# Kernel tuning notes

Measured on AMD Instinct MI355X. Metric: run time of the kernel, lower is better.

## Reference

```python
import jax, jax.numpy as jnp
import numpy as np

INF = 1e38  # matches torch module's INF = 1e+38


def setup_inputs() -> dict:
    key = jax.random.key(0)
    k1, k2, k3 = jax.random.split(key, 3)
    n_len, batch, dim = 2048, 4, 512
    # scale query so QK^T logits don't fully saturate the softmax
    query = jax.random.normal(k1, (n_len, batch, dim), dtype=jnp.float32) * 0.05
    W_in = jax.random.normal(k2, (dim, dim), dtype=jnp.float32) * (1.0 / np.sqrt(dim))
    W_out = jax.random.normal(k3, (dim, 2 * dim), dtype=jnp.float32) * (1.0 / np.sqrt(2 * dim))
    return {"query": query, "W_in": W_in, "W_out": W_out}


def reference(query, W_in, W_out):
    # query: [n_len, batch, dim]; torch .t() swaps first two dims -> [batch, n_len, dim]
    q = jnp.transpose(query, (1, 0, 2))
    b, n, d = q.shape
    # attention_type == 'general': linear_in (no bias), y = x @ W^T
    q = jnp.einsum('bnd,ed->bne', q, W_in)
    # scores: [b, n, n]
    scores = jnp.einsum('bnd,bmd->bnm', q, q)
    # mask = triu(ones) INCLUDING diagonal -> set to -INF (row 0 fully masked)
    mask = jnp.triu(jnp.ones((n, n), dtype=bool))
    scores = jnp.where(mask[None, :, :], -INF, scores)
    weights = jax.nn.softmax(scores, axis=-1)  # row 0 becomes uniform (all -INF)
    # manual zero-out of row 0 of the attention weights
    weights = weights.at[:, 0, :].set(0.0)
    mix = jnp.einsum('bnm,bmd->bnd', weights, q)
    combined = jnp.concatenate([mix, q], axis=-1)  # [b, n, 2d]
    out = jnp.einsum('bnk,dk->bnd', combined, W_out)  # linear_out, no bias
    out = jax.nn.selu(out)
    # final .t() -> [n_len, batch, dim]
    return jnp.transpose(out, (1, 0, 2)), weights
```

## Files before the change

### kernel.cpp

```cpp
#include <hip/hip_runtime.h>
#include <hip/hip_bf16.h>

typedef unsigned short u16;
typedef unsigned int u32;

#define BATCH 4
#define NLEN 2048
#define DIM 512
#define LDSK 40

typedef __attribute__((ext_vector_type(8))) __bf16 bf16x8;
typedef __attribute__((ext_vector_type(4))) float f32x4;

typedef const __attribute__((address_space(1))) void gv_t;
typedef __attribute__((address_space(3))) void lv_t;

__device__ __forceinline__ u16 f32_to_bf16(float f) {
  union { float f; u32 u; } v; v.f = f;
  u32 u = v.u;
  return (u16)((u + 0x7FFFu + ((u >> 16) & 1u)) >> 16);
}
__device__ __forceinline__ u32 pk2(float lo, float hi) {
  return (u32)f32_to_bf16(lo) | ((u32)f32_to_bf16(hi) << 16);
}
__device__ __forceinline__ void stage8_f32(u16* dst, const float* src) {
  float4 a = *(const float4*)src;
  float4 b = *(const float4*)(src + 4);
  uint4 o;
  o.x = pk2(a.x, a.y); o.y = pk2(a.z, a.w);
  o.z = pk2(b.x, b.y); o.w = pk2(b.z, b.w);
  *(uint4*)dst = o;
}
__device__ __forceinline__ void stage16_f32(u16* dst, const float* src) {
  stage8_f32(dst, src); stage8_f32(dst + 8, src + 8);
}
__device__ __forceinline__ u32 addpk_bf16(u32 a, u32 b) {
  float a0 = __uint_as_float(a << 16), a1 = __uint_as_float(a & 0xffff0000u);
  float b0 = __uint_as_float(b << 16), b1 = __uint_as_float(b & 0xffff0000u);
  return pk2(a0 + b0, a1 + b1);
}

template <int NRPW>
__device__ __forceinline__ void glds_rows(const u16* gsrc, size_t gstride, u16* lds,
                                          int wrow0, int lane) {
  const int r = lane >> 3;
  const int c = (lane & 7) * 8;
#pragma unroll
  for (int i = 0; i < NRPW; i += 8) {
    const int row = wrow0 + i + r;
    __builtin_amdgcn_global_load_lds((gv_t*)(gsrc + (size_t)row * gstride + c),
                                     (lv_t*)(lds + row * 64 + c), 16, 0, 0);
  }
}

__global__ __launch_bounds__(256) void k_qproj(const float* __restrict__ query,
                                               const float* __restrict__ W_in,
                                               u16* __restrict__ qp, u16* __restrict__ qt) {
  __shared__ u16 As[64 * LDSK];
  __shared__ u16 Bs[128 * LDSK];
  __shared__ u16 tbuf[128][72];
  const int t = threadIdx.x;
  const int lane = t & 63, wid = t >> 6;
  const int wm = (wid >> 1) * 32, wn = (wid & 1) * 64;
  const int lr = lane & 15, lk = (lane >> 4) * 8;
  const int trow4 = t >> 2, tseg = (t & 3) * 8;
  const int trow2 = t >> 1, thalf = (t & 1) * 16;
  const int rbase = blockIdx.y * 64;
  const int cbase = blockIdx.x * 128;
  const int rg = rbase + trow4;
  const int bb = rg >> 11, nn = rg & 2047;
  const float* aRow = query + (size_t)(nn * BATCH + bb) * DIM + tseg;
  const float* bRow = W_in + (size_t)(cbase + trow2) * DIM + thalf;
  f32x4 acc[2][4] = {};
  for (int k0 = 0; k0 < DIM; k0 += 32) {
    stage8_f32(As + trow4 * LDSK + tseg, aRow + k0);
    stage16_f32(Bs + trow2 * LDSK + thalf, bRow + k0);
    __syncthreads();
    bf16x8 af[2], bfr[4];
#pragma unroll
    for (int m = 0; m < 2; ++m) af[m] = *(const bf16x8*)(As + (wm + m * 16 + lr) * LDSK + lk);
#pragma unroll
    for (int n = 0; n < 4; ++n) bfr[n] = *(const bf16x8*)(Bs + (wn + n * 16 + lr) * LDSK + lk);
#pragma unroll
    for (int m = 0; m < 2; ++m)
#pragma unroll
      for (int n = 0; n < 4; ++n)
        acc[m][n] = __builtin_amdgcn_mfma_f32_16x16x32_bf16(af[m], bfr[n], acc[m][n], 0, 0, 0);
    __syncthreads();
  }
#pragma unroll
  for (int m = 0; m < 2; ++m)
#pragma unroll
    for (int n = 0; n < 4; ++n)
#pragma unroll
      for (int j = 0; j < 4; ++j) {
        int rl = wm + m * 16 + (lane >> 4) * 4 + j;
        int cl = wn + n * 16 + lr;
        u16 v = f32_to_bf16(acc[m][n][j]);
        qp[(size_t)(rbase + rl) * DIM + cbase + cl] = v;
        tbuf[cl][rl] = v;
      }
  __syncthreads();
  const int bb0 = rbase >> 11, nbase = rbase & 2047;
#pragma unroll
  for (int i = 0; i < 4; ++i) {
    int idx = t + i * 256;
    int dl = idx >> 3, c = idx & 7;
    uint4 v = *(const uint4*)&tbuf[dl][c * 8];
    *(uint4*)(qt + (size_t)(bb0 * DIM + cbase + dl) * NLEN + nbase + c * 8) = v;
  }
}

__global__ __launch_bounds__(256) void k_scores(const u16* __restrict__ qp,
                                                u16* __restrict__ swf,
                                                float* __restrict__ spart) {
  const int tri = blockIdx.x;
  const int b = blockIdx.y;
  int nt = 0, cacc = 0;
  while (cacc + nt + 1 <= tri) { cacc += nt + 1; ++nt; }
  const int mt = tri - cacc;
  __shared__ u16 As[128 * 64];
  __shared__ u16 Bs[128 * 64];
  __shared__ float ssum[128][2];
  const int t = threadIdx.x;
  const int lane = t & 63, wid = t >> 6;
  const int wm = (wid >> 1) * 64, wn = (wid & 1) * 64;
  const int lr = lane & 15, lk = (lane >> 4) * 8;
  const u16* ag = qp + (size_t)(b * NLEN + nt * 128) * DIM;
  const u16* bg = qp + (size_t)(b * NLEN + mt * 128) * DIM;
  f32x4 acc[4][4] = {};
  for (int k0 = 0; k0 < DIM; k0 += 64) {
    glds_rows<32>(ag + k0, DIM, As, wid * 32, lane);
    glds_rows<32>(bg + k0, DIM, Bs, wid * 32, lane);
    __syncthreads();
#pragma unroll
    for (int kk = 0; kk < 64; kk += 32) {
      bf16x8 af[4], bfr[4];
#pragma unroll
      for (int m = 0; m < 4; ++m) af[m] = *(const bf16x8*)(As + (wm + m * 16 + lr) * 64 + kk + lk);
#pragma unroll
      for (int n = 0; n < 4; ++n) bfr[n] = *(const bf16x8*)(Bs + (wn + n * 16 + lr) * 64 + kk + lk);
#pragma unroll
      for (int m = 0; m < 4; ++m)
#pragma unroll
        for (int n = 0; n < 4; ++n)
          acc[m][n] = __builtin_amdgcn_mfma_f32_16x16x32_bf16(af[m], bfr[n], acc[m][n], 0, 0, 0);
    }
    __syncthreads();
  }
  u16* wtile = swf + ((size_t)(b * 136 + tri) << 14);
  float rs[4][4];
#pragma unroll
  for (int m = 0; m < 4; ++m)
#pragma unroll
    for (int j = 0; j < 4; ++j) rs[m][j] = 0.f;
#pragma unroll
  for (int m = 0; m < 4; ++m)
#pragma unroll
    for (int n = 0; n < 4; ++n)
#pragma unroll
      for (int j = 0; j < 4; ++j) {
        int rl = wm + m * 16 + (lane >> 4) * 4 + j;
        int cl = wn + n * 16 + lr;
        bool valid = (mt * 128 + cl) < (nt * 128 + rl);
        float e = valid ? __expf(acc[m][n][j]) : 0.f;
        wtile[rl * 128 + cl] = f32_to_bf16(e);
        rs[m][j] += e;
      }
#pragma unroll
  for (int m = 0; m < 4; ++m)
#pragma unroll
    for (int j = 0; j < 4; ++j) {
      float v = rs[m][j];
      v += __shfl_xor(v, 1);
      v += __shfl_xor(v, 2);
      v += __shfl_xor(v, 4);
      v += __shfl_xor(v, 8);
      if ((lane & 15) == 0) ssum[wm + m * 16 + (lane >> 4) * 4 + j][wid & 1] = v;
    }
  __syncthreads();
  if (t < 128) spart[(size_t)(b * 136 + tri) * 128 + t] = ssum[t][0] + ssum[t][1];
}

__global__ __launch_bounds__(256) void k_wnorm(const u16* __restrict__ swf,
                                               const float* __restrict__ spart,
                                               float* __restrict__ w,
                                               float* __restrict__ rowinv,
                                               const float* __restrict__ W_out,
                                               u16* __restrict__ wob) {
  const int n = blockIdx.x, b = blockIdx.y;
  const int t = threadIdx.x;
  if (n >= NLEN) {
    int g = ((n - NLEN) * 4 + b) * 256 + t;
#pragma unroll
    for (int i = 0; i < 4; ++i) {
      int e = g * 32 + i * 8;
      stage8_f32(wob + e, W_out + e);
    }
    return;
  }
  const int nt = n >> 7;
  const int tri0 = nt * (nt + 1) / 2;
  float s = 0.f;
  for (int mt = 0; mt <= nt; ++mt)
    s += spart[(size_t)(b * 136 + tri0 + mt) * 128 + (n & 127)];
  const float inv = (n == 0) ? 0.f : 1.0f / s;
  if (t == 0) rowinv[b * NLEN + n] = inv;
  float* wrow = w + ((size_t)b * NLEN + n) * NLEN;
  const int c8 = t * 8;
  float4 o0 = {0, 0, 0, 0}, o1 = {0, 0, 0, 0};
  if (c8 < (nt + 1) * 128) {
    const int mt = c8 >> 7;
    uint4 rv = *(const uint4*)(swf + ((size_t)(b * 136 + tri0 + mt) << 14) +
                               ((size_t)(n & 127) << 7) + (c8 & 127));
    o0.x = __uint_as_float(rv.x << 16) * inv;
    o0.y = __uint_as_float(rv.x & 0xffff0000u) * inv;
    o0.z = __uint_as_float(rv.y << 16) * inv;
    o0.w = __uint_as_float(rv.y & 0xffff0000u) * inv;
    o1.x = __uint_as_float(rv.z << 16) * inv;
    o1.y = __uint_as_float(rv.z & 0xffff0000u) * inv;
    o1.z = __uint_as_float(rv.w << 16) * inv;
    o1.w = __uint_as_float(rv.w & 0xffff0000u) * inv;
  }
  ((float4*)wrow)[t * 2] = o0;
  ((float4*)wrow)[t * 2 + 1] = o1;
}

__global__ __launch_bounds__(256) void k_mix(const u16* __restrict__ swf,
                                             const u16* __restrict__ qt,
                                             const float* __restrict__ rowinv,
                                             u16* __restrict__ amix,
                                             u16* __restrict__ mix1) {
  const int j = blockIdx.x >> 4;
  const int bdt = blockIdx.x & 15;
  const int b = bdt >> 2, dt = bdt & 3;
  int nt, kt0, ktn, slot;
  if (j < 16) {
    nt = 15 - (j >> 1);
    if ((j & 1) == 0) { kt0 = 0; ktn = 8; slot = 0; }
    else { kt0 = 8; ktn = nt + 1; slot = 1; }
  } else {
    nt = 23 - j; kt0 = 0; ktn = nt + 1; slot = 0;
  }
  __shared__ u16 As[128 * 64];
  __shared__ u16 Bs[128 * 64];
  const int t = threadIdx.x;
  const int lane = t & 63, wid = t >> 6;
  const int wm = (wid >> 1) * 64, wn = (wid & 1) * 64;
  const int lr = lane & 15, lk = (lane >> 4) * 8;
  const size_t tribase = (size_t)(b * 136 + nt * (nt + 1) / 2) << 14;
  const u16* bgbase = qt + (size_t)(b * DIM + dt * 128) * NLEN;
  f32x4 acc[4][4] = {};
  for (int ks = kt0 * 2; ks < ktn * 2; ++ks) {
    const u16* ag = swf + tribase + ((size_t)(ks >> 1) << 14) + (ks & 1) * 64;
    glds_rows<32>(ag, 128, As, wid * 32, lane);
    glds_rows<32>(bgbase + ks * 64, NLEN, Bs, wid * 32, lane);
    __syncthreads();
#pragma unroll
    for (int kk = 0; kk < 64; kk += 32) {
      bf16x8 af[4], bfr[4];
#pragma unroll
      for (int m = 0; m < 4; ++m) af[m] = *(const bf16x8*)(As + (wm + m * 16 + lr) * 64 + kk + lk);
#pragma unroll
      for (int n = 0; n < 4; ++n) bfr[n] = *(const bf16x8*)(Bs + (wn + n * 16 + lr) * 64 + kk + lk);
#pragma unroll
      for (int m = 0; m < 4; ++m)
#pragma unroll
        for (int n = 0; n < 4; ++n)
          acc[m][n] = __builtin_amdgcn_mfma_f32_16x16x32_bf16(af[m], bfr[n], acc[m][n], 0, 0, 0);
    }
    __syncthreads();
  }
  u16* dst = slot ? mix1 : amix;
#pragma unroll
  for (int m = 0; m < 4; ++m)
#pragma unroll
    for (int j2 = 0; j2 < 4; ++j2) {
      int row = nt * 128 + wm + m * 16 + (lane >> 4) * 4 + j2;
      float inv = rowinv[b * NLEN + row];
#pragma unroll
      for (int n = 0; n < 4; ++n) {
        int col = dt * 128 + wn + n * 16 + lr;
        dst[(size_t)(b * NLEN + row) * DIM + col] = f32_to_bf16(acc[m][n][j2] * inv);
      }
    }
}

__global__ __launch_bounds__(256) void k_fold(u16* __restrict__ amix,
                                              const u16* __restrict__ mix1) {
  const int t = threadIdx.x;
#pragma unroll
  for (int i = 0; i < 2; ++i) {
    int g = (blockIdx.x * 2 + i) * 256 + t;
    int rowlin = g >> 6, within = g & 63;
    int b = rowlin >> 10, n = 1024 + (rowlin & 1023);
    size_t off = ((size_t)(b * NLEN + n) * DIM) + within * 8;
    uint4 a = *(const uint4*)(amix + off);
    uint4 c = *(const uint4*)(mix1 + off);
    uint4 o;
    o.x = addpk_bf16(a.x, c.x); o.y = addpk_bf16(a.y, c.y);
    o.z = addpk_bf16(a.z, c.z); o.w = addpk_bf16(a.w, c.w);
    *(uint4*)(amix + off) = o;
  }
}

__global__ __launch_bounds__(256) void k_out(const u16* __restrict__ amix,
                                             const u16* __restrict__ qp,
                                             const u16* __restrict__ wob,
                                             float* __restrict__ out) {
  __shared__ u16 As[128 * 64];
  __shared__ u16 Bs[64 * 64];
  const int bid = blockIdx.x;
  const int et = (bid >> 3) & 7;
  const int rt = ((bid >> 6) << 3) | (bid & 7);
  const int t = threadIdx.x;
  const int lane = t & 63, wid = t >> 6;
  const int wm = (wid >> 1) * 64, wn = (wid & 1) * 32;
  const int lr = lane & 15, lk = (lane >> 4) * 8;
  const int rbase = rt * 128;
  const u16* aMix = amix + (size_t)rbase * DIM;
  const u16* aQ = qp + (size_t)rbase * DIM;
  const u16* bW = wob + (size_t)(et * 64) * (2 * DIM);
  f32x4 acc[4][2] = {};
  for (int k0 = 0; k0 < 2 * DIM; k0 += 64) {
    const u16* ag = (k0 < DIM) ? (aMix + k0) : (aQ + (k0 - DIM));
    glds_rows<32>(ag, DIM, As, wid * 32, lane);
    glds_rows<16>(bW + k0, 2 * DIM, Bs, wid * 16, lane);
    __syncthreads();
#pragma unroll
    for (int kk = 0; kk < 64; kk += 32) {
      bf16x8 af[4], bfr[2];
#pragma unroll
      for (int m = 0; m < 4; ++m) af[m] = *(const bf16x8*)(As + (wm + m * 16 + lr) * 64 + kk + lk);
#pragma unroll
      for (int n = 0; n < 2; ++n) bfr[n] = *(const bf16x8*)(Bs + (wn + n * 16 + lr) * 64 + kk + lk);
#pragma unroll
      for (int m = 0; m < 4; ++m)
#pragma unroll
        for (int n = 0; n < 2; ++n)
          acc[m][n] = __builtin_amdgcn_mfma_f32_16x16x32_bf16(af[m], bfr[n], acc[m][n], 0, 0, 0);
    }
    __syncthreads();
  }
  const float sc = 1.0507009873554805f;
  const float al = 1.6732632423543772f;
#pragma unroll
  for (int m = 0; m < 4; ++m)
#pragma unroll
    for (int n = 0; n < 2; ++n)
#pragma unroll
      for (int j = 0; j < 4; ++j) {
        int row = rbase + wm + m * 16 + (lane >> 4) * 4 + j;
        int col = et * 64 + wn + n * 16 + lr;
        int b2 = row >> 11, n2 = row & 2047;
        float v = acc[m][n][j];
        v = (v > 0.f) ? sc * v : sc * al * (__expf(v) - 1.f);
        out[(size_t)(n2 * BATCH + b2) * DIM + col] = v;
      }
}

extern "C" void kernel_launch(void* const* d_in, const int* in_sizes, int n_in,
                              void* d_out, int out_size, void* d_ws, size_t ws_size,
                              hipStream_t stream) {
  const float* query = (const float*)d_in[0];
  const float* W_in = (const float*)d_in[1];
  const float* W_out = (const float*)d_in[2];
  float* out0 = (float*)d_out;
  float* w = out0 + (size_t)NLEN * BATCH * DIM;

  const size_t PSZ = (size_t)BATCH * NLEN * DIM;
  u16* qp = (u16*)d_ws;
  u16* qt = qp + PSZ;
  u16* amix = qt + PSZ;
  u16* mix1 = amix + PSZ;
  u16* swf = mix1 + PSZ;
  u16* wob = swf + (size_t)BATCH * 136 * 16384;
  float* spart = (float*)(wob + (size_t)DIM * 2 * DIM);
  float* rowinv = spart + (size_t)BATCH * 136 * 128;

  dim3 blk(256);
  k_qproj<<<dim3(DIM / 128, (BATCH * NLEN) / 64), blk, 0, stream>>>(query, W_in, qp, qt);
  k_scores<<<dim3(136, BATCH), blk, 0, stream>>>(qp, swf, spart);
  k_wnorm<<<dim3(NLEN + 16, BATCH), blk, 0, stream>>>(swf, spart, w, rowinv, W_out, wob);
  k_mix<<<dim3(384), blk, 0, stream>>>(swf, qt, rowinv, amix, mix1);
  k_fold<<<dim3(512), blk, 0, stream>>>(amix, mix1);
  k_out<<<dim3(512), blk, 0, stream>>>(amix, qp, wob, out0);
}
```

Baseline: 127.2 us.

## Pre-convert weights to bf16, retile qproj, merge weight normalization into output kernel

Adds a kernel that converts W_in and W_out to bf16 up front. The Q projection is retiled to 128x64 tiles with 64-wide K steps, and the W_in tile is loaded straight into LDS. The separate normalization kernel is removed: k_mix now computes its own per-row inverse sums from spart, and the attention-weight write is folded into the output GEMM launch as extra blocks. This cuts a kernel launch and the rowinv round trip, and lets the memory-bound weight write overlap the output GEMM, at the cost of an extra conversion launch and redundant row-sum work.

```diff
diff --git a/kernel.cpp b/kernel.cpp
--- a/kernel.cpp
+++ b/kernel.cpp
@@ -7,7 +7,6 @@
 #define BATCH 4
 #define NLEN 2048
 #define DIM 512
-#define LDSK 40
 
 typedef __attribute__((ext_vector_type(8))) __bf16 bf16x8;
 typedef __attribute__((ext_vector_type(4))) float f32x4;
@@ -31,9 +30,6 @@
   o.z = pk2(b.x, b.y); o.w = pk2(b.z, b.w);
   *(uint4*)dst = o;
 }
-__device__ __forceinline__ void stage16_f32(u16* dst, const float* src) {
-  stage8_f32(dst, src); stage8_f32(dst + 8, src + 8);
-}
 __device__ __forceinline__ u32 addpk_bf16(u32 a, u32 b) {
   float a0 = __uint_as_float(a << 16), a1 = __uint_as_float(a & 0xffff0000u);
   float b0 = __uint_as_float(b << 16), b1 = __uint_as_float(b & 0xffff0000u);
@@ -53,45 +49,64 @@
   }
 }
 
+__global__ __launch_bounds__(256) void k_conv(const float* __restrict__ W_in,
+                                              const float* __restrict__ W_out,
+                                              u16* __restrict__ wib, u16* __restrict__ wob) {
+  const int NWI = DIM * DIM / 8;
+  int g = blockIdx.x * 768 + threadIdx.x;
+#pragma unroll
+  for (int i = 0; i < 3; ++i, g += 256) {
+    if (g < NWI) stage8_f32(wib + (size_t)g * 8, W_in + (size_t)g * 8);
+    else {
+      int e = g - NWI;
+      stage8_f32(wob + (size_t)e * 8, W_out + (size_t)e * 8);
+    }
+  }
+}
+
 __global__ __launch_bounds__(256) void k_qproj(const float* __restrict__ query,
-                                               const float* __restrict__ W_in,
+                                               const u16* __restrict__ wib,
                                                u16* __restrict__ qp, u16* __restrict__ qt) {
-  __shared__ u16 As[64 * LDSK];
-  __shared__ u16 Bs[128 * LDSK];
-  __shared__ u16 tbuf[128][72];
+  __shared__ u16 As[128 * 64];
+  __shared__ u16 Bs[64 * 64];
+  __shared__ u16 tbuf[64][136];
   const int t = threadIdx.x;
   const int lane = t & 63, wid = t >> 6;
-  const int wm = (wid >> 1) * 32, wn = (wid & 1) * 64;
+  const int wm = (wid >> 1) * 64, wn = (wid & 1) * 32;
   const int lr = lane & 15, lk = (lane >> 4) * 8;
-  const int trow4 = t >> 2, tseg = (t & 3) * 8;
-  const int trow2 = t >> 1, thalf = (t & 1) * 16;
-  const int rbase = blockIdx.y * 64;
-  const int cbase = blockIdx.x * 128;
-  const int rg = rbase + trow4;
-  const int bb = rg >> 11, nn = rg & 2047;
-  const float* aRow = query + (size_t)(nn * BATCH + bb) * DIM + tseg;
-  const float* bRow = W_in + (size_t)(cbase + trow2) * DIM + thalf;
-  f32x4 acc[2][4] = {};
-  for (int k0 = 0; k0 < DIM; k0 += 32) {
-    stage8_f32(As + trow4 * LDSK + tseg, aRow + k0);
-    stage16_f32(Bs + trow2 * LDSK + thalf, bRow + k0);
-    __syncthreads();
-    bf16x8 af[2], bfr[4];
-#pragma unroll
-    for (int m = 0; m < 2; ++m) af[m] = *(const bf16x8*)(As + (wm + m * 16 + lr) * LDSK + lk);
-#pragma unroll
-    for (int n = 0; n < 4; ++n) bfr[n] = *(const bf16x8*)(Bs + (wn + n * 16 + lr) * LDSK + lk);
-#pragma unroll
-    for (int m = 0; m < 2; ++m)
-#pragma unroll
-      for (int n = 0; n < 4; ++n)
-        acc[m][n] = __builtin_amdgcn_mfma_f32_16x16x32_bf16(af[m], bfr[n], acc[m][n], 0, 0, 0);
-    __syncthreads();
-  }
-#pragma unroll
-  for (int m = 0; m < 2; ++m)
-#pragma unroll
-    for (int n = 0; n < 4; ++n)
+  const int et = blockIdx.x;
+  const int rt = blockIdx.y;
+  const int rbase = rt * 128, cbase = et * 64;
+  const int b0 = rbase >> 11, nbase = rbase & 2047;
+  const int tr2 = t >> 1, tc32 = (t & 1) * 32;
+  const int nn = nbase + tr2;
+  const float* aRow = query + (size_t)(nn * BATCH + b0) * DIM + tc32;
+  f32x4 acc[4][2] = {};
+  for (int k0 = 0; k0 < DIM; k0 += 64) {
+#pragma unroll
+    for (int i = 0; i < 4; ++i)
+      stage8_f32(As + tr2 * 64 + tc32 + i * 8, aRow + k0 + i * 8);
+    glds_rows<16>(wib + (size_t)cbase * DIM + k0, DIM, Bs, wid * 16, lane);
+    __syncthreads();
+#pragma unroll
+    for (int kk = 0; kk < 64; kk += 32) {
+      bf16x8 af[4], bfr[2];
+#pragma unroll
+      for (int m = 0; m < 4; ++m) af[m] = *(const bf16x8*)(As + (wm + m * 16 + lr) * 64 + kk + lk);
+#pragma unroll
+      for (int n = 0; n < 2; ++n) bfr[n] = *(const bf16x8*)(Bs + (wn + n * 16 + lr) * 64 + kk + lk);
+#pragma unroll
+      for (int m = 0; m < 4; ++m)
+#pragma unroll
+        for (int n = 0; n < 2; ++n)
+          acc[m][n] = __builtin_amdgcn_mfma_f32_16x16x32_bf16(af[m], bfr[n], acc[m][n], 0, 0, 0);
+    }
+    __syncthreads();
+  }
+#pragma unroll
+  for (int m = 0; m < 4; ++m)
+#pragma unroll
+    for (int n = 0; n < 2; ++n)
 #pragma unroll
       for (int j = 0; j < 4; ++j) {
         int rl = wm + m * 16 + (lane >> 4) * 4 + j;
@@ -101,13 +116,12 @@
         tbuf[cl][rl] = v;
       }
   __syncthreads();
-  const int bb0 = rbase >> 11, nbase = rbase & 2047;
 #pragma unroll
   for (int i = 0; i < 4; ++i) {
     int idx = t + i * 256;
-    int dl = idx >> 3, c = idx & 7;
+    int dl = idx >> 4, c = idx & 15;
     uint4 v = *(const uint4*)&tbuf[dl][c * 8];
-    *(uint4*)(qt + (size_t)(bb0 * DIM + cbase + dl) * NLEN + nbase + c * 8) = v;
+    *(uint4*)(qt + (size_t)(b0 * DIM + cbase + dl) * NLEN + nbase + c * 8) = v;
   }
 }
 
@@ -182,53 +196,9 @@
   if (t < 128) spart[(size_t)(b * 136 + tri) * 128 + t] = ssum[t][0] + ssum[t][1];
 }
 
-__global__ __launch_bounds__(256) void k_wnorm(const u16* __restrict__ swf,
-                                               const float* __restrict__ spart,
-                                               float* __restrict__ w,
-                                               float* __restrict__ rowinv,
-                                               const float* __restrict__ W_out,
-                                               u16* __restrict__ wob) {
-  const int n = blockIdx.x, b = blockIdx.y;
-  const int t = threadIdx.x;
-  if (n >= NLEN) {
-    int g = ((n - NLEN) * 4 + b) * 256 + t;
-#pragma unroll
-    for (int i = 0; i < 4; ++i) {
-      int e = g * 32 + i * 8;
-      stage8_f32(wob + e, W_out + e);
-    }
-    return;
-  }
-  const int nt = n >> 7;
-  const int tri0 = nt * (nt + 1) / 2;
-  float s = 0.f;
-  for (int mt = 0; mt <= nt; ++mt)
-    s += spart[(size_t)(b * 136 + tri0 + mt) * 128 + (n & 127)];
-  const float inv = (n == 0) ? 0.f : 1.0f / s;
-  if (t == 0) rowinv[b * NLEN + n] = inv;
-  float* wrow = w + ((size_t)b * NLEN + n) * NLEN;
-  const int c8 = t * 8;
-  float4 o0 = {0, 0, 0, 0}, o1 = {0, 0, 0, 0};
-  if (c8 < (nt + 1) * 128) {
-    const int mt = c8 >> 7;
-    uint4 rv = *(const uint4*)(swf + ((size_t)(b * 136 + tri0 + mt) << 14) +
-                               ((size_t)(n & 127) << 7) + (c8 & 127));
-    o0.x = __uint_as_float(rv.x << 16) * inv;
-    o0.y = __uint_as_float(rv.x & 0xffff0000u) * inv;
-    o0.z = __uint_as_float(rv.y << 16) * inv;
-    o0.w = __uint_as_float(rv.y & 0xffff0000u) * inv;
-    o1.x = __uint_as_float(rv.z << 16) * inv;
-    o1.y = __uint_as_float(rv.z & 0xffff0000u) * inv;
-    o1.z = __uint_as_float(rv.w << 16) * inv;
-    o1.w = __uint_as_float(rv.w & 0xffff0000u) * inv;
-  }
-  ((float4*)wrow)[t * 2] = o0;
-  ((float4*)wrow)[t * 2 + 1] = o1;
-}
-
 __global__ __launch_bounds__(256) void k_mix(const u16* __restrict__ swf,
                                              const u16* __restrict__ qt,
-                                             const float* __restrict__ rowinv,
+                                             const float* __restrict__ spart,
                                              u16* __restrict__ amix,
                                              u16* __restrict__ mix1) {
   const int j = blockIdx.x >> 4;
@@ -244,11 +214,13 @@
   }
   __shared__ u16 As[128 * 64];
   __shared__ u16 Bs[128 * 64];
+  __shared__ float linv[128];
   const int t = threadIdx.x;
   const int lane = t & 63, wid = t >> 6;
   const int wm = (wid >> 1) * 64, wn = (wid & 1) * 64;
   const int lr = lane & 15, lk = (lane >> 4) * 8;
-  const size_t tribase = (size_t)(b * 136 + nt * (nt + 1) / 2) << 14;
+  const int tri0 = nt * (nt + 1) / 2;
+  const size_t tribase = (size_t)(b * 136 + tri0) << 14;
   const u16* bgbase = qt + (size_t)(b * DIM + dt * 128) * NLEN;
   f32x4 acc[4][4] = {};
   for (int ks = kt0 * 2; ks < ktn * 2; ++ks) {
@@ -271,13 +243,21 @@
     }
     __syncthreads();
   }
+  if (t < 128) {
+    float s = 0.f;
+    for (int mt2 = 0; mt2 <= nt; ++mt2)
+      s += spart[(size_t)(b * 136 + tri0 + mt2) * 128 + t];
+    linv[t] = (nt * 128 + t == 0) ? 0.f : 1.0f / s;
+  }
+  __syncthreads();
   u16* dst = slot ? mix1 : amix;
 #pragma unroll
   for (int m = 0; m < 4; ++m)
 #pragma unroll
     for (int j2 = 0; j2 < 4; ++j2) {
-      int row = nt * 128 + wm + m * 16 + (lane >> 4) * 4 + j2;
-      float inv = rowinv[b * NLEN + row];
+      int rl = wm + m * 16 + (lane >> 4) * 4 + j2;
+      int row = nt * 128 + rl;
+      float inv = linv[rl];
 #pragma unroll
       for (int n = 0; n < 4; ++n) {
         int col = dt * 128 + wn + n * 16 + lr;
@@ -304,16 +284,48 @@
   }
 }
 
-__global__ __launch_bounds__(256) void k_out(const u16* __restrict__ amix,
-                                             const u16* __restrict__ qp,
-                                             const u16* __restrict__ wob,
-                                             float* __restrict__ out) {
+__global__ __launch_bounds__(256) void k_outw(const u16* __restrict__ amix,
+                                              const u16* __restrict__ qp,
+                                              const u16* __restrict__ wob,
+                                              const u16* __restrict__ swf,
+                                              const float* __restrict__ spart,
+                                              float* __restrict__ out,
+                                              float* __restrict__ w) {
   __shared__ u16 As[128 * 64];
   __shared__ u16 Bs[64 * 64];
   const int bid = blockIdx.x;
+  const int t = threadIdx.x;
+  if (bid >= 512) {
+    const int r = bid - 512;
+    const int b = r >> 11, n = r & 2047;
+    const int nt = n >> 7;
+    const int tri0 = nt * (nt + 1) / 2;
+    float s = 0.f;
+    for (int mt = 0; mt <= nt; ++mt)
+      s += spart[(size_t)(b * 136 + tri0 + mt) * 128 + (n & 127)];
+    const float inv = (n == 0) ? 0.f : 1.0f / s;
+    float* wrow = w + ((size_t)b * NLEN + n) * NLEN;
+    const int c8 = t * 8;
+    float4 o0 = {0, 0, 0, 0}, o1 = {0, 0, 0, 0};
+    if (c8 < (nt + 1) * 128) {
+      const int mt = c8 >> 7;
+      uint4 rv = *(const uint4*)(swf + ((size_t)(b * 136 + tri0 + mt) << 14) +
+                                 ((size_t)(n & 127) << 7) + (c8 & 127));
+      o0.x = __uint_as_float(rv.x << 16) * inv;
+      o0.y = __uint_as_float(rv.x & 0xffff0000u) * inv;
+      o0.z = __uint_as_float(rv.y << 16) * inv;
+      o0.w = __uint_as_float(rv.y & 0xffff0000u) * inv;
+      o1.x = __uint_as_float(rv.z << 16) * inv;
+      o1.y = __uint_as_float(rv.z & 0xffff0000u) * inv;
+      o1.z = __uint_as_float(rv.w << 16) * inv;
+      o1.w = __uint_as_float(rv.w & 0xffff0000u) * inv;
+    }
+    ((float4*)wrow)[t * 2] = o0;
+    ((float4*)wrow)[t * 2 + 1] = o1;
+    return;
+  }
   const int et = (bid >> 3) & 7;
   const int rt = ((bid >> 6) << 3) | (bid & 7);
-  const int t = threadIdx.x;
   const int lane = t & 63, wid = t >> 6;
   const int wm = (wid >> 1) * 64, wn = (wid & 1) * 32;
   const int lr = lane & 15, lk = (lane >> 4) * 8;
@@ -374,15 +386,15 @@
   u16* amix = qt + PSZ;
   u16* mix1 = amix + PSZ;
   u16* swf = mix1 + PSZ;
-  u16* wob = swf + (size_t)BATCH * 136 * 16384;
+  u16* wib = swf + (size_t)BATCH * 136 * 16384;
+  u16* wob = wib + (size_t)DIM * DIM;
   float* spart = (float*)(wob + (size_t)DIM * 2 * DIM);
-  float* rowinv = spart + (size_t)BATCH * 136 * 128;
 
   dim3 blk(256);
-  k_qproj<<<dim3(DIM / 128, (BATCH * NLEN) / 64), blk, 0, stream>>>(query, W_in, qp, qt);
+  k_conv<<<dim3(128), blk, 0, stream>>>(W_in, W_out, wib, wob);
+  k_qproj<<<dim3(8, 64), blk, 0, stream>>>(query, wib, qp, qt);
   k_scores<<<dim3(136, BATCH), blk, 0, stream>>>(qp, swf, spart);
-  k_wnorm<<<dim3(NLEN + 16, BATCH), blk, 0, stream>>>(swf, spart, w, rowinv, W_out, wob);
-  k_mix<<<dim3(384), blk, 0, stream>>>(swf, qt, rowinv, amix, mix1);
+  k_mix<<<dim3(384), blk, 0, stream>>>(swf, qt, spart, amix, mix1);
   k_fold<<<dim3(512), blk, 0, stream>>>(amix, mix1);
-  k_out<<<dim3(512), blk, 0, stream>>>(amix, qp, wob, out0);
-}
+  k_outw<<<dim3(512 + BATCH * NLEN), blk, 0, stream>>>(amix, qp, wob, swf, spart, out0, w);
+}
```

Result: slower. 135.9 us (+6.8%).
